# Performance work log

Hardware: AMD Instinct MI355X
Metric: run time of the kernel (lower is better)

Reference implementation:

```python
import jax, jax.numpy as jnp
from jax import lax
import numpy as np

B, T, UNITS, OUT_STEPS, NUM_FEAT, BINS, DF = 512, 1024, 256, 32, 32, 32, 15

# Acklam rational approximation of the inverse normal CDF (numpy, only used to
# build the constant Student-t quantile boundaries, replacing scipy.stats.t.ppf).
def _norm_ppf(p):
    p = np.asarray(p, dtype=np.float64)
    a = [-3.969683028665376e+01, 2.209460984245205e+02, -2.759285104469687e+02,
         1.383577518672690e+02, -3.066479806614716e+01, 2.506628277459239e+00]
    b = [-5.447609879822406e+01, 1.615858368580409e+02, -1.556989798598866e+02,
         6.680131188771972e+01, -1.328068155288572e+01]
    c = [-7.784894002430293e-03, -3.223964580411365e-01, -2.400758277161838e+00,
         -2.549732539343734e+00, 4.374664141464968e+00, 2.938163982698783e+00]
    d = [7.784695709041462e-03, 3.224671290700398e-01, 2.445134137142996e+00,
         3.754408661907416e+00]
    x = np.empty_like(p)
    lo, hi = 0.02425, 1.0 - 0.02425
    m = p < lo
    q = np.sqrt(-2.0 * np.log(p[m]))
    x[m] = (((((c[0]*q+c[1])*q+c[2])*q+c[3])*q+c[4])*q+c[5]) / ((((d[0]*q+d[1])*q+d[2])*q+d[3])*q+1.0)
    m = (p >= lo) & (p <= hi)
    q = p[m] - 0.5
    r = q * q
    x[m] = (((((a[0]*r+a[1])*r+a[2])*r+a[3])*r+a[4])*r+a[5])*q / (((((b[0]*r+b[1])*r+b[2])*r+b[3])*r+b[4])*r+1.0)
    m = p > hi
    q = np.sqrt(-2.0 * np.log(1.0 - p[m]))
    x[m] = -(((((c[0]*q+c[1])*q+c[2])*q+c[3])*q+c[4])*q+c[5]) / ((((d[0]*q+d[1])*q+d[2])*q+d[3])*q+1.0)
    return x

# Cornish-Fisher expansion of the Student-t inverse CDF around the normal quantile.
def _t_ppf(p, df):
    z = _norm_ppf(p)
    g1 = (z**3 + z) / 4.0
    g2 = (5*z**5 + 16*z**3 + 3*z) / 96.0
    g3 = (3*z**7 + 19*z**5 + 17*z**3 - 15*z) / 384.0
    g4 = (79*z**9 + 776*z**7 + 1482*z**5 - 1920*z**3 - 945*z) / 92160.0
    return z + g1/df + g2/df**2 + g3/df**3 + g4/df**4

_T_BASE = _t_ppf(np.linspace(0.0001, 0.9999, BINS - 1), DF).astype(np.float32)  # [BINS-1]


def _lstm_step(kernel, rec_kernel, bias, h, c, x):
    # Keras LSTMCell: gate order i|f|g|o, sigmoid gates, tanh cell activation.
    z = x @ kernel + h @ rec_kernel + bias
    i, f, g, o = jnp.split(z, 4, axis=-1)
    c = jax.nn.sigmoid(f) * c + jax.nn.sigmoid(i) * jnp.tanh(g)
    h = jax.nn.sigmoid(o) * jnp.tanh(c)
    return h, c


def reference(inputs, kernel, rec_kernel, bias, dense_w, dense_b):
    mu = jnp.mean(inputs, axis=1, keepdims=True)    # [B,1,1]
    sigma = jnp.std(inputs, axis=1, keepdims=True)  # [B,1,1] population std (tf.reduce_std)
    base = jnp.asarray(_T_BASE)                     # [BINS-1]
    bounds = base[None, :] * sigma[:, 0, 0, None] + mu[:, 0, 0, None]  # [B,BINS-1], sorted
    x = inputs[:, :, 0]                             # [B,T]
    # Vectorized bucketization (replaces tf.map_fn + tft.apply_buckets).
    idx = jax.vmap(lambda xb, bb: jnp.searchsorted(bb, xb, side='right'))(x, bounds)  # [B,T]
    hist = jax.nn.one_hot(idx, BINS, dtype=inputs.dtype)  # [B,T,BINS]

    units = kernel.shape[1] // 4
    h0 = jnp.zeros((x.shape[0], units), inputs.dtype)

    def enc(carry, xt):
        h, c = _lstm_step(kernel, rec_kernel, bias, carry[0], carry[1], xt)
        return (h, c), None

    (h, c), _ = lax.scan(enc, (h0, h0), hist.transpose(1, 0, 2))  # warmup over T steps
    pred = jax.nn.softmax(h @ dense_w + dense_b)                   # [B,NUM_FEAT]

    def dec(carry, _):
        h, c, p = carry
        h, c = _lstm_step(kernel, rec_kernel, bias, h, c, p)
        p = jax.nn.softmax(h @ dense_w + dense_b)
        return (h, c, p), p

    _, rest = lax.scan(dec, (h, c, pred), None, length=OUT_STEPS - 1)
    preds = jnp.concatenate([pred[None], rest], axis=0)  # [OUT_STEPS,B,F]
    preds = preds.transpose(1, 0, 2)[:, :, None, :]      # [B,OUT_STEPS,1,F]
    return preds, mu, sigma


def setup_inputs():
    key = jax.random.key(0)
    ks = jax.random.split(key, 4)
    return {
        "inputs": jax.random.normal(ks[0], (B, T, 1), jnp.float32),
        "kernel": jax.random.normal(ks[1], (BINS, 4 * UNITS), jnp.float32) * 0.1,
        "rec_kernel": jax.random.normal(ks[2], (UNITS, 4 * UNITS), jnp.float32) * 0.1,
        "bias": jnp.zeros((4 * UNITS,), jnp.float32),
        "dense_w": jax.random.normal(ks[3], (UNITS, NUM_FEAT), jnp.float32) * 0.1,
        "dense_b": jnp.zeros((NUM_FEAT,), jnp.float32),
    }
```

## Files before the change

### kernel.cpp

```cpp
#include <hip/hip_runtime.h>
#include <math.h>

#define TT      1024
#define BATCH   512
#define UNITSN  256
#define ZDIM    1024
#define NFEAT   32
#define OSTEPS  32
#define NBND    31
#define OUT_MU  (BATCH*OSTEPS*NFEAT)
#define OUT_SG  (OUT_MU + BATCH)

#define NQR     22
#define NQL     10
#define HQS     36
#define HQ(buf,row,reg) ((((buf)*2+(row))*2+(reg))*HQS)

__device__ __forceinline__ float sigm(float x)  { return 1.0f / (1.0f + __expf(-x)); }
__device__ __forceinline__ float ftanh(float x) { float e = __expf(2.0f * x); return 1.0f - 2.0f / (e + 1.0f); }

__device__ __forceinline__ int dot4i8(unsigned int a, unsigned int b, int c) {
#if __has_builtin(__builtin_amdgcn_sdot4)
    return __builtin_amdgcn_sdot4((int)a, (int)b, c, false);
#else
    int r = c;
    #pragma unroll
    for (int i = 0; i < 4; ++i) {
        r += (int)(signed char)(a >> (8*i)) * (int)(signed char)(b >> (8*i));
    }
    return r;
#endif
}

__global__ void k_tbase(float* __restrict__ tb) {
    int i = threadIdx.x;
    if (i >= NBND) return;
    double step = (0.9999 - 0.0001) / 30.0;
    double p = 0.0001 + (double)i * step;
    if (i == 30) p = 0.9999;

    const double a0=-39.69683028665376, a1=220.9460984245205, a2=-275.9285104469687,
                 a3=138.357751867269,   a4=-30.66479806614716, a5=2.506628277459239;
    const double b0=-54.47609879822406, b1=161.5858368580409, b2=-155.6989798598866,
                 b3=66.80131188771972,  b4=-13.28068155288572;
    const double c0=-0.007784894002430293, c1=-0.3223964580411365, c2=-2.400758277161838,
                 c3=-2.549732539343734,    c4=4.374664141464968,   c5=2.938163982698783;
    const double d0=0.007784695709041462,  d1=0.3224671290700398,  d2=2.445134137142996,
                 d3=3.754408661907416;
    const double lo = 0.02425, hi = 1.0 - 0.02425;
    double z;
    if (p < lo) {
        double q = sqrt(-2.0 * log(p));
        z = (((((c0*q+c1)*q+c2)*q+c3)*q+c4)*q+c5) / ((((d0*q+d1)*q+d2)*q+d3)*q+1.0);
    } else if (p <= hi) {
        double q = p - 0.5;
        double r = q*q;
        z = (((((a0*r+a1)*r+a2)*r+a3)*r+a4)*r+a5)*q /
            (((((b0*r+b1)*r+b2)*r+b3)*r+b4)*r+1.0);
    } else {
        double q = sqrt(-2.0 * log(1.0 - p));
        z = -((((((c0*q+c1)*q+c2)*q+c3)*q+c4)*q+c5) / ((((d0*q+d1)*q+d2)*q+d3)*q+1.0));
    }
    double z2=z*z, z3=z2*z, z5=z3*z2, z7=z5*z2, z9=z7*z2;
    double g1=(z3+z)/4.0;
    double g2=(5.0*z5+16.0*z3+3.0*z)/96.0;
    double g3=(3.0*z7+19.0*z5+17.0*z3-15.0*z)/384.0;
    double g4=(79.0*z9+776.0*z7+1482.0*z5-1920.0*z3-945.0*z)/92160.0;
    const double df = 15.0;
    double t = z + g1/df + g2/(df*df) + g3/(df*df*df) + g4/(df*df*df*df);
    tb[i] = (float)t;
}

__global__ __launch_bounds__(1024)
void k_musig(const float* __restrict__ x, float* __restrict__ out,
             float* __restrict__ muv, float* __restrict__ sgv) {
    int b = blockIdx.x;
    int t = threadIdx.x;
    __shared__ float red[16];
    __shared__ float sMu;
    float v = x[(size_t)b * TT + t];

    float s = v;
    #pragma unroll
    for (int o = 32; o >= 1; o >>= 1) { s += __shfl_xor(s, o, 64); }
    int wid = t >> 6, lane = t & 63;
    if (lane == 0) red[wid] = s;
    __syncthreads();
    if (t == 0) {
        float tot = 0.f;
        for (int w = 0; w < 16; ++w) tot += red[w];
        sMu = tot * (1.0f / 1024.0f);
    }
    __syncthreads();
    float mu = sMu;
    float d = v - mu;
    s = d * d;
    #pragma unroll
    for (int o = 32; o >= 1; o >>= 1) { s += __shfl_xor(s, o, 64); }
    if (lane == 0) red[wid] = s;
    __syncthreads();
    if (t == 0) {
        float tot = 0.f;
        for (int w = 0; w < 16; ++w) tot += red[w];
        float sg = sqrtf(tot * (1.0f / 1024.0f));
        out[OUT_MU + b] = mu;
        out[OUT_SG + b] = sg;
        muv[b] = mu;
        sgv[b] = sg;
    }
}

__global__ __launch_bounds__(256)
void k_scales(const float* __restrict__ Rec, float* __restrict__ SW,
              float* __restrict__ SInv) {
    int j = blockIdx.x * 256 + threadIdx.x;
    float m = 0.f;
    for (int k = 0; k < 256; ++k) m = fmaxf(m, fabsf(Rec[(size_t)k * ZDIM + j]));
    SW[j]   = m * (1.0f / 16129.0f);
    SInv[j] = (m > 0.f) ? (127.0f / m) : 0.f;
}

__global__ __launch_bounds__(256)
void k_packQ(const float* __restrict__ Rec, const float* __restrict__ SInv,
             uint4* __restrict__ Q) {
    int e = blockIdx.x * 256 + threadIdx.x;
    int s = e >> 9, t = e & 511;
    int u = t >> 1, kh = t & 1;
    int k0 = kh * 128 + s * 4;
    unsigned int d[4];
    #pragma unroll
    for (int g = 0; g < 4; ++g) {
        int j = g * 256 + u;
        float inv = SInv[j];
        unsigned int dw = 0;
        #pragma unroll
        for (int i = 0; i < 4; ++i) {
            int q = __float2int_rn(Rec[(size_t)(k0 + i) * ZDIM + j] * inv);
            dw |= ((unsigned int)(q & 0xff)) << (8 * i);
        }
        d[g] = dw;
    }
    Q[e] = make_uint4(d[0], d[1], d[2], d[3]);
}

__global__ __launch_bounds__(256)
void k_packK(const float* __restrict__ Kmat, const float* __restrict__ Bias,
             float* __restrict__ KB) {
    int e = blockIdx.x * 256 + threadIdx.x;
    int i = e >> 10, c = e & 1023;
    int u = c >> 2, g = c & 3;
    int j = g * 256 + u;
    KB[e] = Kmat[(size_t)i * ZDIM + j] + Bias[j];
}

__global__ __launch_bounds__(512)
void k_lstm15(const float* __restrict__ x,
              const uint4* __restrict__ Q,
              const float* __restrict__ SW,
              const float* __restrict__ KB,
              const float* __restrict__ Dw,
              const float* __restrict__ Db,
              const float* __restrict__ tb,
              const float* __restrict__ muv,
              const float* __restrict__ sgv,
              float* __restrict__ out)
{
    __shared__ uint4 sWq[NQL * 512];
    __shared__ unsigned int sHq[2 * 2 * 2 * HQS];
    __shared__ float sHT[UNITSN][2];
    __shared__ unsigned char sIdx[2][TT];
    __shared__ float sBnd[2][32];
    __shared__ float sPT[NFEAT][2];
    __shared__ float sLog[2][NFEAT];

    const int tid = threadIdx.x;
    const int u   = tid >> 1;
    const int kh  = tid & 1;
    const int b0  = blockIdx.x * 2;

    if (tid < 64) {
        int rr = tid >> 5, j = tid & 31;
        if (j < NBND) sBnd[rr][j] = tb[j] * sgv[b0 + rr] + muv[b0 + rr];
    }
    if (tid < 2 * 2 * 2 * HQS) sHq[tid] = 0u;
    if (tid < UNITSN * 2) ((float*)sHT)[tid] = 0.f;

    uint4 Wreg[NQR];
    #pragma unroll
    for (int j = 0; j < NQR; ++j) {
        uint4 w = Q[j * 512 + tid];
        asm volatile("" : "+v"(w.x), "+v"(w.y), "+v"(w.z), "+v"(w.w));
        Wreg[j] = w;
    }
    #pragma unroll
    for (int l = 0; l < NQL; ++l) {
        sWq[l * 512 + tid] = Q[(NQR + l) * 512 + tid];
    }

    float4 SW4 = make_float4(SW[u], SW[256 + u], SW[512 + u], SW[768 + u]);

    for (int e = tid; e < 2 * TT; e += 512) {
        int rr = e >> 10, t = e & 1023;
        float xv = x[(size_t)(b0 + rr) * TT + t];
        int id = 0;
        #pragma unroll
        for (int q = 0; q < NBND; ++q) { id += (sBnd[rr][q] <= xv) ? 1 : 0; }
        sIdx[rr][t] = (unsigned char)id;
    }
    __syncthreads();

    float cC = 0.f;
    int cur = 0;
    const int wbyte_reg = u >> 7;
    const int wbyte_off = u & 127;

    auto stepCore = [&](float4 kbSelf) {
        const unsigned int* hb0 = &sHq[HQ(cur, 0, kh)];
        const unsigned int* hb1 = &sHq[HQ(cur, 1, kh)];
        int4 A0 = {0, 0, 0, 0}, A1 = {0, 0, 0, 0};
        #pragma unroll
        for (int s4 = 0; s4 < 8; ++s4) {
            uint4 hh0 = *(const uint4*)(hb0 + s4 * 4);
            uint4 hh1 = *(const uint4*)(hb1 + s4 * 4);
            #pragma unroll
            for (int i = 0; i < 4; ++i) {
                const int j = s4 * 4 + i;
                uint4 w = (j < NQR) ? Wreg[(j < NQR) ? j : 0]
                                    : sWq[(j - NQR) * 512 + tid];
                unsigned int h0 = (i==0)?hh0.x:(i==1)?hh0.y:(i==2)?hh0.z:hh0.w;
                unsigned int h1 = (i==0)?hh1.x:(i==1)?hh1.y:(i==2)?hh1.z:hh1.w;
                A0.x = dot4i8(h0, w.x, A0.x); A0.y = dot4i8(h0, w.y, A0.y);
                A0.z = dot4i8(h0, w.z, A0.z); A0.w = dot4i8(h0, w.w, A0.w);
                A1.x = dot4i8(h1, w.x, A1.x); A1.y = dot4i8(h1, w.y, A1.y);
                A1.z = dot4i8(h1, w.z, A1.z); A1.w = dot4i8(h1, w.w, A1.w);
            }
        }
        A0.x += __shfl_xor(A0.x, 1); A0.y += __shfl_xor(A0.y, 1);
        A0.z += __shfl_xor(A0.z, 1); A0.w += __shfl_xor(A0.w, 1);
        A1.x += __shfl_xor(A1.x, 1); A1.y += __shfl_xor(A1.y, 1);
        A1.z += __shfl_xor(A1.z, 1); A1.w += __shfl_xor(A1.w, 1);
        int qi = kh ? A1.x : A0.x;
        int qf = kh ? A1.y : A0.y;
        int qg = kh ? A1.z : A0.z;
        int qo = kh ? A1.w : A0.w;
        float zi = (float)qi * SW4.x + kbSelf.x;
        float zf = (float)qf * SW4.y + kbSelf.y;
        float zg = (float)qg * SW4.z + kbSelf.z;
        float zo = (float)qo * SW4.w + kbSelf.w;
        cC = sigm(zf) * cC + sigm(zi) * ftanh(zg);
        float hv = sigm(zo) * ftanh(cC);
        sHT[u][kh] = hv;
        int qh = __float2int_rn(hv * 127.0f);
        ((unsigned char*)sHq)[(HQ(cur ^ 1, kh, wbyte_reg) << 2) + wbyte_off] =
            (unsigned char)qh;
        cur ^= 1;
        __syncthreads();
    };

    auto softmaxStore = [&](int s) {
        if (tid < 64) {
            int rr = tid >> 5, f = tid & 31;
            float acc = Db[f];
            #pragma unroll 4
            for (int uu = 0; uu < UNITSN; ++uu) {
                acc = fmaf(sHT[uu][rr], Dw[uu * NFEAT + f], acc);
            }
            sLog[rr][f] = acc;
        }
        __syncthreads();
        if (tid < 2) {
            int rr = tid;
            float mx = sLog[rr][0];
            for (int f = 1; f < NFEAT; ++f) mx = fmaxf(mx, sLog[rr][f]);
            float ssum = 0.f;
            for (int f = 0; f < NFEAT; ++f) {
                float e = __expf(sLog[rr][f] - mx);
                sLog[rr][f] = e;
                ssum += e;
            }
            float inv = 1.0f / ssum;
            for (int f = 0; f < NFEAT; ++f) {
                float p = sLog[rr][f] * inv;
                sPT[f][rr] = p;
                out[((size_t)(b0 + rr) * OSTEPS + s) * NFEAT + f] = p;
            }
        }
        __syncthreads();
    };

    #pragma unroll 1
    for (int t = 0; t < TT; ++t) {
        float4 kb = *(const float4*)&KB[((int)sIdx[kh][t] << 10) + (u << 2)];
        stepCore(kb);
    }
    softmaxStore(0);

    #pragma unroll 1
    for (int s = 1; s < OSTEPS; ++s) {
        float4 a0 = make_float4(0.f, 0.f, 0.f, 0.f), a1 = a0;
        #pragma unroll
        for (int ii = 0; ii < 16; ++ii) {
            int i = kh * 16 + ii;
            float4 w = *(const float4*)&KB[(i << 10) + (u << 2)];
            float p0 = sPT[i][0], p1 = sPT[i][1];
            a0.x = fmaf(p0, w.x, a0.x); a0.y = fmaf(p0, w.y, a0.y);
            a0.z = fmaf(p0, w.z, a0.z); a0.w = fmaf(p0, w.w, a0.w);
            a1.x = fmaf(p1, w.x, a1.x); a1.y = fmaf(p1, w.y, a1.y);
            a1.z = fmaf(p1, w.z, a1.z); a1.w = fmaf(p1, w.w, a1.w);
        }
        a0.x += __shfl_xor(a0.x, 1); a0.y += __shfl_xor(a0.y, 1);
        a0.z += __shfl_xor(a0.z, 1); a0.w += __shfl_xor(a0.w, 1);
        a1.x += __shfl_xor(a1.x, 1); a1.y += __shfl_xor(a1.y, 1);
        a1.z += __shfl_xor(a1.z, 1); a1.w += __shfl_xor(a1.w, 1);
        float4 kbSelf = (kh == 0) ? a0 : a1;
        stepCore(kbSelf);
        softmaxStore(s);
    }
}

extern "C" void kernel_launch(void* const* d_in, const int* in_sizes, int n_in,
                              void* d_out, int out_size, void* d_ws, size_t ws_size,
                              hipStream_t stream) {
    const float* inputs = (const float*)d_in[0];
    const float* kernel = (const float*)d_in[1];
    const float* rec    = (const float*)d_in[2];
    const float* bias   = (const float*)d_in[3];
    const float* dw     = (const float*)d_in[4];
    const float* db     = (const float*)d_in[5];
    float* out = (float*)d_out;

    float* tbp  = (float*)d_ws;
    float* muv  = tbp + 64;
    float* sgv  = muv + BATCH;
    float* SW   = (float*)((char*)d_ws + 4352);
    float* SInv = (float*)((char*)d_ws + 8448);
    uint4* Q    = (uint4*)((char*)d_ws + 12544);
    float* KB   = (float*)((char*)d_ws + 12544 + 262144);

    k_tbase<<<1, 32, 0, stream>>>(tbp);
    k_musig<<<BATCH, 1024, 0, stream>>>(inputs, out, muv, sgv);
    k_scales<<<4, 256, 0, stream>>>(rec, SW, SInv);
    k_packQ<<<64, 256, 0, stream>>>(rec, SInv, Q);
    k_packK<<<128, 256, 0, stream>>>(kernel, bias, KB);
    k_lstm15<<<BATCH / 2, 512, 0, stream>>>(inputs, Q, SW, KB, dw, db,
                                            tbp, muv, sgv, out);
}
```

Before: 2.040 ms.

## Process one batch row per block instead of two, doubling grid size

The LSTM kernel now assigns one batch row per 512-thread block and launches BATCH blocks instead of BATCH/2. Each thread accumulates one set of int8 dot products instead of two, which shortens the serial per-step chain, and the extra blocks fill more of the 256 CUs. Because each row is handled separately, every block reloads the recurrent weights, so weight-load traffic doubles and the kernel needs about two waves of blocks. One more weight chunk is kept in registers instead of LDS.

```diff
diff --git a/kernel.cpp b/kernel.cpp
--- a/kernel.cpp
+++ b/kernel.cpp
@@ -11,10 +11,10 @@
 #define OUT_MU  (BATCH*OSTEPS*NFEAT)
 #define OUT_SG  (OUT_MU + BATCH)
 
-#define NQR     22
-#define NQL     10
+#define NQR     23
+#define NQL     9
 #define HQS     36
-#define HQ(buf,row,reg) ((((buf)*2+(row))*2+(reg))*HQS)
+#define HQ(buf,reg) (((buf)*2+(reg))*HQS)
 
 __device__ __forceinline__ float sigm(float x)  { return 1.0f / (1.0f + __expf(-x)); }
 __device__ __forceinline__ float ftanh(float x) { float e = __expf(2.0f * x); return 1.0f - 2.0f / (e + 1.0f); }
@@ -154,7 +154,7 @@
 }
 
 __global__ __launch_bounds__(512)
-void k_lstm15(const float* __restrict__ x,
+void k_lstm16(const float* __restrict__ x,
               const uint4* __restrict__ Q,
               const float* __restrict__ SW,
               const float* __restrict__ KB,
@@ -166,24 +166,23 @@
               float* __restrict__ out)
 {
     __shared__ uint4 sWq[NQL * 512];
-    __shared__ unsigned int sHq[2 * 2 * 2 * HQS];
-    __shared__ float sHT[UNITSN][2];
-    __shared__ unsigned char sIdx[2][TT];
-    __shared__ float sBnd[2][32];
-    __shared__ float sPT[NFEAT][2];
-    __shared__ float sLog[2][NFEAT];
+    __shared__ unsigned int sHq[2 * 2 * HQS];
+    __shared__ float sHT[UNITSN];
+    __shared__ unsigned char sIdx[TT];
+    __shared__ float sBnd[32];
+    __shared__ float sPT[NFEAT];
+    __shared__ float sLog[NFEAT];
 
     const int tid = threadIdx.x;
     const int u   = tid >> 1;
     const int kh  = tid & 1;
-    const int b0  = blockIdx.x * 2;
-
-    if (tid < 64) {
-        int rr = tid >> 5, j = tid & 31;
-        if (j < NBND) sBnd[rr][j] = tb[j] * sgv[b0 + rr] + muv[b0 + rr];
-    }
-    if (tid < 2 * 2 * 2 * HQS) sHq[tid] = 0u;
-    if (tid < UNITSN * 2) ((float*)sHT)[tid] = 0.f;
+    const int row = blockIdx.x;
+
+    if (tid < 32) {
+        if (tid < NBND) sBnd[tid] = tb[tid] * sgv[row] + muv[row];
+    }
+    if (tid < 2 * 2 * HQS) sHq[tid] = 0u;
+    if (tid < UNITSN) sHT[tid] = 0.f;
 
     uint4 Wreg[NQR];
     #pragma unroll
@@ -199,13 +198,12 @@
 
     float4 SW4 = make_float4(SW[u], SW[256 + u], SW[512 + u], SW[768 + u]);
 
-    for (int e = tid; e < 2 * TT; e += 512) {
-        int rr = e >> 10, t = e & 1023;
-        float xv = x[(size_t)(b0 + rr) * TT + t];
+    for (int t = tid; t < TT; t += 512) {
+        float xv = x[(size_t)row * TT + t];
         int id = 0;
         #pragma unroll
-        for (int q = 0; q < NBND; ++q) { id += (sBnd[rr][q] <= xv) ? 1 : 0; }
-        sIdx[rr][t] = (unsigned char)id;
+        for (int q = 0; q < NBND; ++q) { id += (sBnd[q] <= xv) ? 1 : 0; }
+        sIdx[t] = (unsigned char)id;
     }
     __syncthreads();
 
@@ -215,74 +213,64 @@
     const int wbyte_off = u & 127;
 
     auto stepCore = [&](float4 kbSelf) {
-        const unsigned int* hb0 = &sHq[HQ(cur, 0, kh)];
-        const unsigned int* hb1 = &sHq[HQ(cur, 1, kh)];
-        int4 A0 = {0, 0, 0, 0}, A1 = {0, 0, 0, 0};
+        const unsigned int* hb = &sHq[HQ(cur, kh)];
+        int4 A = {0, 0, 0, 0};
         #pragma unroll
         for (int s4 = 0; s4 < 8; ++s4) {
-            uint4 hh0 = *(const uint4*)(hb0 + s4 * 4);
-            uint4 hh1 = *(const uint4*)(hb1 + s4 * 4);
+            uint4 hh = *(const uint4*)(hb + s4 * 4);
             #pragma unroll
             for (int i = 0; i < 4; ++i) {
                 const int j = s4 * 4 + i;
                 uint4 w = (j < NQR) ? Wreg[(j < NQR) ? j : 0]
                                     : sWq[(j - NQR) * 512 + tid];
-                unsigned int h0 = (i==0)?hh0.x:(i==1)?hh0.y:(i==2)?hh0.z:hh0.w;
-                unsigned int h1 = (i==0)?hh1.x:(i==1)?hh1.y:(i==2)?hh1.z:hh1.w;
-                A0.x = dot4i8(h0, w.x, A0.x); A0.y = dot4i8(h0, w.y, A0.y);
-                A0.z = dot4i8(h0, w.z, A0.z); A0.w = dot4i8(h0, w.w, A0.w);
-                A1.x = dot4i8(h1, w.x, A1.x); A1.y = dot4i8(h1, w.y, A1.y);
-                A1.z = dot4i8(h1, w.z, A1.z); A1.w = dot4i8(h1, w.w, A1.w);
+                unsigned int h0 = (i==0)?hh.x:(i==1)?hh.y:(i==2)?hh.z:hh.w;
+                A.x = dot4i8(h0, w.x, A.x); A.y = dot4i8(h0, w.y, A.y);
+                A.z = dot4i8(h0, w.z, A.z); A.w = dot4i8(h0, w.w, A.w);
             }
         }
-        A0.x += __shfl_xor(A0.x, 1); A0.y += __shfl_xor(A0.y, 1);
-        A0.z += __shfl_xor(A0.z, 1); A0.w += __shfl_xor(A0.w, 1);
-        A1.x += __shfl_xor(A1.x, 1); A1.y += __shfl_xor(A1.y, 1);
-        A1.z += __shfl_xor(A1.z, 1); A1.w += __shfl_xor(A1.w, 1);
-        int qi = kh ? A1.x : A0.x;
-        int qf = kh ? A1.y : A0.y;
-        int qg = kh ? A1.z : A0.z;
-        int qo = kh ? A1.w : A0.w;
-        float zi = (float)qi * SW4.x + kbSelf.x;
-        float zf = (float)qf * SW4.y + kbSelf.y;
-        float zg = (float)qg * SW4.z + kbSelf.z;
-        float zo = (float)qo * SW4.w + kbSelf.w;
+        A.x += __shfl_xor(A.x, 1); A.y += __shfl_xor(A.y, 1);
+        A.z += __shfl_xor(A.z, 1); A.w += __shfl_xor(A.w, 1);
+        float zi = (float)A.x * SW4.x + kbSelf.x;
+        float zf = (float)A.y * SW4.y + kbSelf.y;
+        float zg = (float)A.z * SW4.z + kbSelf.z;
+        float zo = (float)A.w * SW4.w + kbSelf.w;
         cC = sigm(zf) * cC + sigm(zi) * ftanh(zg);
         float hv = sigm(zo) * ftanh(cC);
-        sHT[u][kh] = hv;
-        int qh = __float2int_rn(hv * 127.0f);
-        ((unsigned char*)sHq)[(HQ(cur ^ 1, kh, wbyte_reg) << 2) + wbyte_off] =
-            (unsigned char)qh;
+        if (kh == 0) {
+            sHT[u] = hv;
+            int qh = __float2int_rn(hv * 127.0f);
+            ((unsigned char*)sHq)[(HQ(cur ^ 1, wbyte_reg) << 2) + wbyte_off] =
+                (unsigned char)qh;
+        }
         cur ^= 1;
         __syncthreads();
     };
 
     auto softmaxStore = [&](int s) {
-        if (tid < 64) {
-            int rr = tid >> 5, f = tid & 31;
+        if (tid < NFEAT) {
+            int f = tid;
             float acc = Db[f];
             #pragma unroll 4
             for (int uu = 0; uu < UNITSN; ++uu) {
-                acc = fmaf(sHT[uu][rr], Dw[uu * NFEAT + f], acc);
+                acc = fmaf(sHT[uu], Dw[uu * NFEAT + f], acc);
             }
-            sLog[rr][f] = acc;
+            sLog[f] = acc;
         }
         __syncthreads();
-        if (tid < 2) {
-            int rr = tid;
-            float mx = sLog[rr][0];
-            for (int f = 1; f < NFEAT; ++f) mx = fmaxf(mx, sLog[rr][f]);
+        if (tid == 0) {
+            float mx = sLog[0];
+            for (int f = 1; f < NFEAT; ++f) mx = fmaxf(mx, sLog[f]);
             float ssum = 0.f;
             for (int f = 0; f < NFEAT; ++f) {
-                float e = __expf(sLog[rr][f] - mx);
-                sLog[rr][f] = e;
+                float e = __expf(sLog[f] - mx);
+                sLog[f] = e;
                 ssum += e;
             }
             float inv = 1.0f / ssum;
             for (int f = 0; f < NFEAT; ++f) {
-                float p = sLog[rr][f] * inv;
-                sPT[f][rr] = p;
-                out[((size_t)(b0 + rr) * OSTEPS + s) * NFEAT + f] = p;
+                float p = sLog[f] * inv;
+                sPT[f] = p;
+                out[((size_t)row * OSTEPS + s) * NFEAT + f] = p;
             }
         }
         __syncthreads();
@@ -290,30 +278,25 @@
 
     #pragma unroll 1
     for (int t = 0; t < TT; ++t) {
-        float4 kb = *(const float4*)&KB[((int)sIdx[kh][t] << 10) + (u << 2)];
+        float4 kb = *(const float4*)&KB[((int)sIdx[t] << 10) + (u << 2)];
         stepCore(kb);
     }
     softmaxStore(0);
 
     #pragma unroll 1
     for (int s = 1; s < OSTEPS; ++s) {
-        float4 a0 = make_float4(0.f, 0.f, 0.f, 0.f), a1 = a0;
+        float4 a = make_float4(0.f, 0.f, 0.f, 0.f);
         #pragma unroll
         for (int ii = 0; ii < 16; ++ii) {
             int i = kh * 16 + ii;
             float4 w = *(const float4*)&KB[(i << 10) + (u << 2)];
-            float p0 = sPT[i][0], p1 = sPT[i][1];
-            a0.x = fmaf(p0, w.x, a0.x); a0.y = fmaf(p0, w.y, a0.y);
-            a0.z = fmaf(p0, w.z, a0.z); a0.w = fmaf(p0, w.w, a0.w);
-            a1.x = fmaf(p1, w.x, a1.x); a1.y = fmaf(p1, w.y, a1.y);
-            a1.z = fmaf(p1, w.z, a1.z); a1.w = fmaf(p1, w.w, a1.w);
-        }
-        a0.x += __shfl_xor(a0.x, 1); a0.y += __shfl_xor(a0.y, 1);
-        a0.z += __shfl_xor(a0.z, 1); a0.w += __shfl_xor(a0.w, 1);
-        a1.x += __shfl_xor(a1.x, 1); a1.y += __shfl_xor(a1.y, 1);
-        a1.z += __shfl_xor(a1.z, 1); a1.w += __shfl_xor(a1.w, 1);
-        float4 kbSelf = (kh == 0) ? a0 : a1;
-        stepCore(kbSelf);
+            float p = sPT[i];
+            a.x = fmaf(p, w.x, a.x); a.y = fmaf(p, w.y, a.y);
+            a.z = fmaf(p, w.z, a.z); a.w = fmaf(p, w.w, a.w);
+        }
+        a.x += __shfl_xor(a.x, 1); a.y += __shfl_xor(a.y, 1);
+        a.z += __shfl_xor(a.z, 1); a.w += __shfl_xor(a.w, 1);
+        stepCore(a);
         softmaxStore(s);
     }
 }
@@ -342,6 +325,6 @@
     k_scales<<<4, 256, 0, stream>>>(rec, SW, SInv);
     k_packQ<<<64, 256, 0, stream>>>(rec, SInv, Q);
     k_packK<<<128, 256, 0, stream>>>(kernel, bias, KB);
-    k_lstm15<<<BATCH / 2, 512, 0, stream>>>(inputs, Q, SW, KB, dw, db,
-                                            tbp, muv, sgv, out);
-}
+    k_lstm16<<<BATCH, 512, 0, stream>>>(inputs, Q, SW, KB, dw, db,
+                                        tbp, muv, sgv, out);
+}
```

Result: slower. 2.933 ms (+43.7%).
